# Kernel tuning notes

Measured on AMD Instinct MI355X. Metric: run time of the kernel, lower is better.

The kernel has to match this reference:

```python
import jax, jax.numpy as jnp
import numpy as np

N_USER = 100000
N_ITEM = 200000
LATDIM = 64
N_EDGE = 9600000
GNN_LAYERS = 3
N_NODES = N_USER + N_ITEM


def setup_inputs() -> dict:
    key = jax.random.key(0)
    k1, k2, k3, k4, k5 = jax.random.split(key, 5)
    uEmbeds = jax.random.normal(k1, (N_USER, LATDIM), dtype=jnp.float32)
    iEmbeds = jax.random.normal(k2, (N_ITEM, LATDIM), dtype=jnp.float32)
    edge_row = jax.random.randint(k3, (N_EDGE,), 0, N_NODES, dtype=jnp.int64 if jax.config.jax_enable_x64 else jnp.int32)
    edge_col = jax.random.randint(k4, (N_EDGE,), 0, N_NODES, dtype=jnp.int64 if jax.config.jax_enable_x64 else jnp.int32)
    edge_vals = jax.random.uniform(k5, (N_EDGE,), dtype=jnp.float32)
    return {"uEmbeds": uEmbeds, "iEmbeds": iEmbeds,
            "edge_row": edge_row, "edge_col": edge_col, "edge_vals": edge_vals}


def _spmm(edge_row, edge_col, edge_vals, embeds):
    # sparse [N,N] @ dense [N,d] via gather + segment_sum over rows
    msgs = edge_vals[:, None] * embeds[edge_col]  # [E, d]
    return jax.ops.segment_sum(msgs, edge_row, num_segments=N_NODES)


def reference(uEmbeds, iEmbeds, edge_row, edge_col, edge_vals):
    embeds = jnp.concatenate([uEmbeds, iEmbeds], axis=0)  # [N, d]
    acc = embeds
    cur = embeds
    for _ in range(GNN_LAYERS):  # fixed small layer count
        cur = _spmm(edge_row, edge_col, edge_vals, cur)
        acc = acc + cur
    return acc[:N_USER], acc[N_USER:]
```

## Files before the change

### kernel.cpp

```cpp
#include <hip/hip_runtime.h>

#define N_USER 100000
#define N_ITEM 200000
#define N_NODES 300000
#define LATDIM 64
#define N_EDGE 9600000
#define BSHIFT 7
#define RPB 128
#define NBUCK ((N_NODES + RPB - 1) / RPB)
#define NBLK 256
#define EPB (N_EDGE / NBLK)

__device__ __forceinline__ unsigned int pack_bf16x2(float a, float b) {
    unsigned int ua = __float_as_uint(a);
    unsigned int ub = __float_as_uint(b);
    ua = (ua + 0x7fffu + ((ua >> 16) & 1u)) >> 16;
    ub = (ub + 0x7fffu + ((ub >> 16) & 1u)) >> 16;
    return ua | (ub << 16);
}
__device__ __forceinline__ unsigned short f32_to_bf16(float a) {
    unsigned int ua = __float_as_uint(a);
    return (unsigned short)((ua + 0x7fffu + ((ua >> 16) & 1u)) >> 16);
}

__global__ void lgcn_init(const float* __restrict__ u,
                          const float* __restrict__ it,
                          float* __restrict__ out,
                          unsigned int* __restrict__ curp) {
    const size_t total2 = (size_t)N_NODES * 32;
    const size_t u2 = (size_t)N_USER * 32;
    const float2* uu = (const float2*)u;
    const float2* ii = (const float2*)it;
    float2* o2 = (float2*)out;
    for (size_t i = (size_t)blockIdx.x * blockDim.x + threadIdx.x; i < total2;
         i += (size_t)gridDim.x * blockDim.x) {
        float2 v = (i < u2) ? uu[i] : ii[i - u2];
        o2[i] = v;
        curp[i] = pack_bf16x2(v.x, v.y);
    }
}

__global__ void lgcn_bhist(const int* __restrict__ row, int* __restrict__ histBM) {
    __shared__ int h[NBUCK];
    int blk = blockIdx.x;
    for (int i = threadIdx.x; i < NBUCK; i += blockDim.x) h[i] = 0;
    __syncthreads();
    int s = blk * EPB;
    for (int e = s + threadIdx.x; e < s + EPB; e += blockDim.x)
        atomicAdd(&h[row[e] >> BSHIFT], 1);
    __syncthreads();
    for (int i = threadIdx.x; i < NBUCK; i += blockDim.x)
        histBM[(size_t)blk * NBUCK + i] = h[i];
}

__global__ void lgcn_bposscan(const int* __restrict__ histBM,
                              int* __restrict__ posT,
                              int* __restrict__ bucketTotal) {
    __shared__ int s[NBLK];
    int bucket = blockIdx.x;
    int tid = threadIdx.x;
    int v = histBM[(size_t)tid * NBUCK + bucket];
    s[tid] = v;
    __syncthreads();
    for (int o = 1; o < NBLK; o <<= 1) {
        int t = (tid >= o) ? s[tid - o] : 0;
        __syncthreads();
        s[tid] += t;
        __syncthreads();
    }
    posT[(size_t)bucket * NBLK + tid] = s[tid] - v;
    if (tid == NBLK - 1) bucketTotal[bucket] = s[tid];
}

__global__ void lgcn_bscan(const int* __restrict__ bucketTotal,
                           int* __restrict__ bcur, int* __restrict__ rowStart) {
    __shared__ int tsum[1024];
    int tid = threadIdx.x;
    int base = tid * 3;
    int a0 = 0, a1 = 0, a2 = 0;
    if (base < NBUCK) a0 = bucketTotal[base];
    if (base + 1 < NBUCK) a1 = bucketTotal[base + 1];
    if (base + 2 < NBUCK) a2 = bucketTotal[base + 2];
    tsum[tid] = a0 + a1 + a2;
    __syncthreads();
    for (int o = 1; o < 1024; o <<= 1) {
        int t = (tid >= o) ? tsum[tid - o] : 0;
        __syncthreads();
        tsum[tid] += t;
        __syncthreads();
    }
    int excl = (tid > 0) ? tsum[tid - 1] : 0;
    if (base < NBUCK) bcur[base] = excl;
    if (base + 1 < NBUCK) bcur[base + 1] = excl + a0;
    if (base + 2 < NBUCK) bcur[base + 2] = excl + a0 + a1;
    if (tid == 1023) {
        bcur[NBUCK] = N_EDGE;
        rowStart[N_NODES] = N_EDGE;
    }
}

__global__ void lgcn_bplace(const int* __restrict__ row, const int* __restrict__ col,
                            const float* __restrict__ vals,
                            const int* __restrict__ bcur, const int* __restrict__ posT,
                            uint2* __restrict__ recs) {
    __shared__ int cursor[NBUCK];
    int blk = blockIdx.x;
    for (int i = threadIdx.x; i < NBUCK; i += blockDim.x)
        cursor[i] = bcur[i] + posT[(size_t)i * NBLK + blk];
    __syncthreads();
    int s = blk * EPB;
    for (int e = s + threadIdx.x; e < s + EPB; e += blockDim.x) {
        int r = row[e];
        int pos = atomicAdd(&cursor[r >> BSHIFT], 1);
        uint2 rec;
        rec.x = (unsigned int)col[e] | ((unsigned int)(r & (RPB - 1)) << 19);
        rec.y = __float_as_uint(vals[e]);
        recs[pos] = rec;
    }
}

__global__ void lgcn_csr(const int* __restrict__ bcur,
                         const uint2* __restrict__ recs,
                         int* __restrict__ rowStart,
                         int* __restrict__ colS, unsigned short* __restrict__ valS) {
    __shared__ int rcnt[RPB];
    __shared__ int sc[RPB];
    __shared__ int rcur[RPB];
    int b = blockIdx.x, tid = threadIdx.x;
    int s = bcur[b], e = bcur[b + 1];
    for (int i = tid; i < RPB; i += blockDim.x) rcnt[i] = 0;
    __syncthreads();
    for (int k = s + tid; k < e; k += blockDim.x)
        atomicAdd(&rcnt[recs[k].x >> 19], 1);
    __syncthreads();
    int v = (tid < RPB) ? rcnt[tid] : 0;
    if (tid < RPB) sc[tid] = v;
    __syncthreads();
    for (int o = 1; o < RPB; o <<= 1) {
        int t = (tid < RPB && tid >= o) ? sc[tid - o] : 0;
        __syncthreads();
        if (tid < RPB) sc[tid] += t;
        __syncthreads();
    }
    if (tid < RPB) {
        int excl = s + sc[tid] - v;
        rcur[tid] = excl;
        int r = b * RPB + tid;
        if (r < N_NODES) rowStart[r] = excl;
    }
    __syncthreads();
    for (int k = s + tid; k < e; k += blockDim.x) {
        uint2 rec = recs[k];
        int rl = (int)(rec.x >> 19);
        int pos = atomicAdd(&rcur[rl], 1);
        colS[pos] = (int)(rec.x & 0x7ffffu);
        valS[pos] = f32_to_bf16(__uint_as_float(rec.y));
    }
}

__global__ void lgcn_spmm(const int* __restrict__ rowStart,
                          const int* __restrict__ colS,
                          const unsigned short* __restrict__ valS,
                          const unsigned int* __restrict__ cur,
                          unsigned int* __restrict__ nxt,
                          float* __restrict__ out) {
    int wid = blockIdx.x * (blockDim.x >> 6) + (threadIdx.x >> 6);
    if (wid >= N_NODES) return;
    int lane = threadIdx.x & 63;
    int half = lane >> 5;
    int l32 = lane & 31;
    int s = rowStart[wid];
    int e = rowStart[wid + 1];
    float sx = 0.f, sy = 0.f, tx = 0.f, ty = 0.f;
    int k = s + half;
    for (; k + 6 < e; k += 8) {
        int c0 = colS[k];
        int c1 = colS[k + 2];
        int c2 = colS[k + 4];
        int c3 = colS[k + 6];
        float v0 = __uint_as_float(((unsigned int)valS[k]) << 16);
        float v1 = __uint_as_float(((unsigned int)valS[k + 2]) << 16);
        float v2 = __uint_as_float(((unsigned int)valS[k + 4]) << 16);
        float v3 = __uint_as_float(((unsigned int)valS[k + 6]) << 16);
        unsigned int p0 = cur[(size_t)c0 * 32 + l32];
        unsigned int p1 = cur[(size_t)c1 * 32 + l32];
        unsigned int p2 = cur[(size_t)c2 * 32 + l32];
        unsigned int p3 = cur[(size_t)c3 * 32 + l32];
        sx += v0 * __uint_as_float(p0 << 16);
        sy += v0 * __uint_as_float(p0 & 0xffff0000u);
        tx += v1 * __uint_as_float(p1 << 16);
        ty += v1 * __uint_as_float(p1 & 0xffff0000u);
        sx += v2 * __uint_as_float(p2 << 16);
        sy += v2 * __uint_as_float(p2 & 0xffff0000u);
        tx += v3 * __uint_as_float(p3 << 16);
        ty += v3 * __uint_as_float(p3 & 0xffff0000u);
    }
    for (; k < e; k += 2) {
        int c = colS[k];
        float v = __uint_as_float(((unsigned int)valS[k]) << 16);
        unsigned int p = cur[(size_t)c * 32 + l32];
        sx += v * __uint_as_float(p << 16);
        sy += v * __uint_as_float(p & 0xffff0000u);
    }
    sx += tx; sy += ty;
    sx += __shfl_xor(sx, 32);
    sy += __shfl_xor(sy, 32);
    if (half == 0) {
        size_t base = (size_t)wid * 32 + l32;
        nxt[base] = pack_bf16x2(sx, sy);
        float2* o2 = (float2*)out;
        float2 t = o2[base];
        t.x += sx;
        t.y += sy;
        o2[base] = t;
    }
}

extern "C" void kernel_launch(void* const* d_in, const int* in_sizes, int n_in,
                              void* d_out, int out_size, void* d_ws, size_t ws_size,
                              hipStream_t stream) {
    const float* uEmb = (const float*)d_in[0];
    const float* iEmb = (const float*)d_in[1];
    const int* erow = (const int*)d_in[2];
    const int* ecol = (const int*)d_in[3];
    const float* evals = (const float*)d_in[4];
    float* out = (float*)d_out;

    char* p = (char*)d_ws;
    const size_t curBytes = (size_t)N_NODES * 32 * sizeof(unsigned int);
    unsigned int* curA = (unsigned int*)p;
    unsigned int* curB = (unsigned int*)(p + curBytes);
    uint2* recs = (uint2*)p;
    p += 2 * curBytes;
    int* colS = (int*)p;
    int* histBM = (int*)p;
    int* posT = (int*)(p + (size_t)NBLK * NBUCK * sizeof(int));
    p += (size_t)N_EDGE * sizeof(int);
    unsigned short* valS = (unsigned short*)p; p += (size_t)N_EDGE * sizeof(unsigned short);
    int* rowStart = (int*)p; p += (size_t)(N_NODES + 1) * sizeof(int);
    int* bcur = (int*)p; p += (size_t)(NBUCK + 1) * sizeof(int);
    int* bucketTotal = (int*)p; p += (size_t)NBUCK * sizeof(int);

    const int T = 256;
    const int G_SPMM = (N_NODES + 3) / 4;

    lgcn_bhist<<<NBLK, T, 0, stream>>>(erow, histBM);
    lgcn_bposscan<<<NBUCK, NBLK, 0, stream>>>(histBM, posT, bucketTotal);
    lgcn_bscan<<<1, 1024, 0, stream>>>(bucketTotal, bcur, rowStart);
    lgcn_bplace<<<NBLK, T, 0, stream>>>(erow, ecol, evals, bcur, posT, recs);
    lgcn_csr<<<NBUCK, T, 0, stream>>>(bcur, recs, rowStart, colS, valS);

    lgcn_init<<<2048, T, 0, stream>>>(uEmb, iEmb, out, curA);

    unsigned int* cur = curA;
    unsigned int* nxt = curB;
    for (int layer = 0; layer < 3; ++layer) {
        lgcn_spmm<<<G_SPMM, T, 0, stream>>>(rowStart, colS, valS, cur, nxt, out);
        unsigned int* t = cur; cur = nxt; nxt = t;
    }
}
```

Before: 1.363 ms.

## Enlarge CSR buckets, use more placement blocks, unroll SpMM gathers to eight

Bucket size grows from 128 to 512 rows and placement blocks from 256 to 1024. The bucket scan now uses one thread per bucket, and the CSR build launches one thread per row in the bucket (512 threads). The SpMM kernel gains an 8-way unrolled gather loop so more independent embedding loads are in flight per wavefront. Together these aim to cut the CSR construction cost and improve memory-level parallelism in the gather. The risks are a larger histogram/posT footprint, a bposscan that now launches 1024 threads per block, and higher register pressure in the SpMM.

```diff
diff --git a/kernel.cpp b/kernel.cpp
--- a/kernel.cpp
+++ b/kernel.cpp
@@ -5,10 +5,10 @@
 #define N_NODES 300000
 #define LATDIM 64
 #define N_EDGE 9600000
-#define BSHIFT 7
-#define RPB 128
+#define BSHIFT 9
+#define RPB 512
 #define NBUCK ((N_NODES + RPB - 1) / RPB)
-#define NBLK 256
+#define NBLK 1024
 #define EPB (N_EDGE / NBLK)
 
 __device__ __forceinline__ unsigned int pack_bf16x2(float a, float b) {
@@ -76,12 +76,8 @@
                            int* __restrict__ bcur, int* __restrict__ rowStart) {
     __shared__ int tsum[1024];
     int tid = threadIdx.x;
-    int base = tid * 3;
-    int a0 = 0, a1 = 0, a2 = 0;
-    if (base < NBUCK) a0 = bucketTotal[base];
-    if (base + 1 < NBUCK) a1 = bucketTotal[base + 1];
-    if (base + 2 < NBUCK) a2 = bucketTotal[base + 2];
-    tsum[tid] = a0 + a1 + a2;
+    int v = (tid < NBUCK) ? bucketTotal[tid] : 0;
+    tsum[tid] = v;
     __syncthreads();
     for (int o = 1; o < 1024; o <<= 1) {
         int t = (tid >= o) ? tsum[tid - o] : 0;
@@ -89,11 +85,8 @@
         tsum[tid] += t;
         __syncthreads();
     }
-    int excl = (tid > 0) ? tsum[tid - 1] : 0;
-    if (base < NBUCK) bcur[base] = excl;
-    if (base + 1 < NBUCK) bcur[base + 1] = excl + a0;
-    if (base + 2 < NBUCK) bcur[base + 2] = excl + a0 + a1;
-    if (tid == 1023) {
+    if (tid < NBUCK) bcur[tid] = tsum[tid] - v;
+    if (tid == 0) {
         bcur[NBUCK] = N_EDGE;
         rowStart[N_NODES] = N_EDGE;
     }
@@ -128,21 +121,21 @@
     __shared__ int rcur[RPB];
     int b = blockIdx.x, tid = threadIdx.x;
     int s = bcur[b], e = bcur[b + 1];
-    for (int i = tid; i < RPB; i += blockDim.x) rcnt[i] = 0;
+    rcnt[tid] = 0;
     __syncthreads();
     for (int k = s + tid; k < e; k += blockDim.x)
         atomicAdd(&rcnt[recs[k].x >> 19], 1);
     __syncthreads();
-    int v = (tid < RPB) ? rcnt[tid] : 0;
-    if (tid < RPB) sc[tid] = v;
+    int v = rcnt[tid];
+    sc[tid] = v;
     __syncthreads();
     for (int o = 1; o < RPB; o <<= 1) {
-        int t = (tid < RPB && tid >= o) ? sc[tid - o] : 0;
-        __syncthreads();
-        if (tid < RPB) sc[tid] += t;
-        __syncthreads();
-    }
-    if (tid < RPB) {
+        int t = (tid >= o) ? sc[tid - o] : 0;
+        __syncthreads();
+        sc[tid] += t;
+        __syncthreads();
+    }
+    {
         int excl = s + sc[tid] - v;
         rcur[tid] = excl;
         int r = b * RPB + tid;
@@ -173,6 +166,48 @@
     int e = rowStart[wid + 1];
     float sx = 0.f, sy = 0.f, tx = 0.f, ty = 0.f;
     int k = s + half;
+    for (; k + 14 < e; k += 16) {
+        int c0 = colS[k];
+        int c1 = colS[k + 2];
+        int c2 = colS[k + 4];
+        int c3 = colS[k + 6];
+        int c4 = colS[k + 8];
+        int c5 = colS[k + 10];
+        int c6 = colS[k + 12];
+        int c7 = colS[k + 14];
+        unsigned int p0 = cur[(size_t)c0 * 32 + l32];
+        unsigned int p1 = cur[(size_t)c1 * 32 + l32];
+        unsigned int p2 = cur[(size_t)c2 * 32 + l32];
+        unsigned int p3 = cur[(size_t)c3 * 32 + l32];
+        unsigned int p4 = cur[(size_t)c4 * 32 + l32];
+        unsigned int p5 = cur[(size_t)c5 * 32 + l32];
+        unsigned int p6 = cur[(size_t)c6 * 32 + l32];
+        unsigned int p7 = cur[(size_t)c7 * 32 + l32];
+        float v0 = __uint_as_float(((unsigned int)valS[k]) << 16);
+        float v1 = __uint_as_float(((unsigned int)valS[k + 2]) << 16);
+        float v2 = __uint_as_float(((unsigned int)valS[k + 4]) << 16);
+        float v3 = __uint_as_float(((unsigned int)valS[k + 6]) << 16);
+        float v4 = __uint_as_float(((unsigned int)valS[k + 8]) << 16);
+        float v5 = __uint_as_float(((unsigned int)valS[k + 10]) << 16);
+        float v6 = __uint_as_float(((unsigned int)valS[k + 12]) << 16);
+        float v7 = __uint_as_float(((unsigned int)valS[k + 14]) << 16);
+        sx += v0 * __uint_as_float(p0 << 16);
+        sy += v0 * __uint_as_float(p0 & 0xffff0000u);
+        tx += v1 * __uint_as_float(p1 << 16);
+        ty += v1 * __uint_as_float(p1 & 0xffff0000u);
+        sx += v2 * __uint_as_float(p2 << 16);
+        sy += v2 * __uint_as_float(p2 & 0xffff0000u);
+        tx += v3 * __uint_as_float(p3 << 16);
+        ty += v3 * __uint_as_float(p3 & 0xffff0000u);
+        sx += v4 * __uint_as_float(p4 << 16);
+        sy += v4 * __uint_as_float(p4 & 0xffff0000u);
+        tx += v5 * __uint_as_float(p5 << 16);
+        ty += v5 * __uint_as_float(p5 & 0xffff0000u);
+        sx += v6 * __uint_as_float(p6 << 16);
+        sy += v6 * __uint_as_float(p6 & 0xffff0000u);
+        tx += v7 * __uint_as_float(p7 << 16);
+        ty += v7 * __uint_as_float(p7 & 0xffff0000u);
+    }
     for (; k + 6 < e; k += 8) {
         int c0 = colS[k];
         int c1 = colS[k + 2];
@@ -248,7 +283,7 @@
     lgcn_bposscan<<<NBUCK, NBLK, 0, stream>>>(histBM, posT, bucketTotal);
     lgcn_bscan<<<1, 1024, 0, stream>>>(bucketTotal, bcur, rowStart);
     lgcn_bplace<<<NBLK, T, 0, stream>>>(erow, ecol, evals, bcur, posT, recs);
-    lgcn_csr<<<NBUCK, T, 0, stream>>>(bcur, recs, rowStart, colS, valS);
+    lgcn_csr<<<NBUCK, RPB, 0, stream>>>(bcur, recs, rowStart, colS, valS);
 
     lgcn_init<<<2048, T, 0, stream>>>(uEmb, iEmb, out, curA);
 
```

New measurement: 1.247 ms. 1.09x faster.
